# Optimization experiments

Hardware: AMD Instinct MI355X
Metric: run time of the kernel (lower is better)

The kernel has to match this reference:

```python
import jax, jax.numpy as jnp
import numpy as np

CAPACITY = 1_000_000
IN_FEATURES = 64
OUT_FEATURES = 64


def setup_inputs() -> dict:
    key = jax.random.key(0)
    k1, k2, k3 = jax.random.split(key, 3)
    query = jax.random.normal(k1, (IN_FEATURES,), dtype=jnp.float32)
    keys = jax.random.normal(k2, (CAPACITY, IN_FEATURES), dtype=jnp.float32)
    values = jax.random.normal(k3, (CAPACITY, OUT_FEATURES), dtype=jnp.float32)
    return {"query": query, "keys": keys, "values": values}


def reference(query, keys, values):
    # attention: [capacity] = keys [C, Din] @ query [Din]
    scores = keys @ query
    attention = jax.nn.softmax(scores, axis=0)
    # out: [Dout] = attention [C] @ values [C, Dout]
    out = attention @ values
    # usage-tracking argmax (softmax is monotone, argmax of scores == argmax of attention)
    amax = jnp.argmax(scores)
    return out, amax
```

## Files before the change

kernel.cpp:

```cpp
#include <hip/hip_runtime.h>
#include <math.h>

#define C_CAP 1000000
#define DIM 64

#define SCORES_OFF 0
#define P1_OFF     1000000
#define HDR_OFF    1010000
#define ACC_OFF    1010064

#define NB1 1024
#define NW1 (NB1 * 4)
#define NT64 (C_CAP / 64)
#define NB3 2048
#define NW3 (NB3 * 4)
#define NCHUNKS (C_CAP / 64)

__global__ __launch_bounds__(256, 4) void nd_scores(
    const float* __restrict__ query,
    const float* __restrict__ keys,
    float* __restrict__ ws, int ntiles, int stride)
{
    const int tid  = threadIdx.x;
    const int lane = tid & 63;
    const int wave = tid >> 6;
    const int wglobal = blockIdx.x * 4 + wave;

    float qs[64];
    #pragma unroll
    for (int j = 0; j < 64; ++j)
        qs[j] = __uint_as_float(__builtin_amdgcn_readfirstlane(__float_as_uint(query[j])));

    float m = -1e30f, l = 0.f;

    for (int t = wglobal; t < ntiles; t += stride) {
        const float4* __restrict__ kp =
            (const float4*)(keys + ((size_t)t * 64 + lane) * 64);

        float a0 = 0.f, a1 = 0.f, a2 = 0.f, a3 = 0.f;
        #pragma unroll
        for (int j = 0; j < 16; ++j) {
            const float4 k = kp[j];
            a0 = fmaf(k.x, qs[4 * j + 0], a0);
            a1 = fmaf(k.y, qs[4 * j + 1], a1);
            a2 = fmaf(k.z, qs[4 * j + 2], a2);
            a3 = fmaf(k.w, qs[4 * j + 3], a3);
        }
        const float s = (a0 + a1) + (a2 + a3);

        ws[SCORES_OFF + t * 64 + lane] = s;
        l += __expf(s);
        m = fmaxf(m, s);
    }

    #pragma unroll
    for (int off = 1; off <= 32; off <<= 1) {
        l += __shfl_xor(l, off);
        m = fmaxf(m, __shfl_xor(m, off));
    }

    __shared__ float s_m[4], s_l[4];
    if (lane == 0) { s_m[wave] = m; s_l[wave] = l; }
    __syncthreads();
    if (tid == 0) {
        float bm = s_m[0], bl = s_l[0];
        #pragma unroll
        for (int wv = 1; wv < 4; ++wv) {
            bl += s_l[wv];
            bm = fmaxf(bm, s_m[wv]);
        }
        float* bp = ws + P1_OFF + (size_t)blockIdx.x * 4;
        bp[0] = bm;
        bp[1] = bl;
    }
}

__global__ __launch_bounds__(256) void nd_reduce(float* __restrict__ ws, int nb)
{
    const int tid = threadIdx.x;
    float m = -1e30f, l = 0.f;
    for (int b = tid; b < nb; b += 256) {
        const float* bp = ws + P1_OFF + (size_t)b * 4;
        l += bp[1];
        m = fmaxf(m, bp[0]);
    }
    __shared__ float sm[256], sl[256];
    sm[tid] = m; sl[tid] = l;
    __syncthreads();
    for (int s = 128; s > 0; s >>= 1) {
        if (tid < s) {
            sl[tid] += sl[tid + s];
            sm[tid] = fmaxf(sm[tid], sm[tid + s]);
        }
        __syncthreads();
    }
    if (tid == 0) {
        const float M = sm[0];
        ws[HDR_OFF + 0] = M;
        ws[HDR_OFF + 1] = sl[0] * __expf(-M);
        ((int*)ws)[HDR_OFF + 2] = 0;
    }
    if (tid < 64) ws[ACC_OFF + tid] = 0.f;
}

__global__ __launch_bounds__(256, 8) void nd_pv(
    const float* __restrict__ values,
    float* __restrict__ ws, int nchunks, int nwaves_total)
{
    const int tid  = threadIdx.x;
    const int lane = tid & 63;
    const int wave = tid >> 6;
    const int wglobal = blockIdx.x * 4 + wave;

    const float M   = ws[HDR_OFF];
    const float thr = M - 23.0f;
    float acc = 0.f;

    for (int c = wglobal; c < nchunks; c += nwaves_total) {
        const float s = ws[SCORES_OFF + (size_t)c * 64 + lane];
        unsigned long long mask = __ballot(s > thr);
        if (mask) {
            if (s == M) ((int*)ws)[HDR_OFF + 2] = c * 64 + lane;
            const float w = __expf(s - M);
            while (mask) {
                const int b = __ffsll((long long)mask) - 1;
                mask &= mask - 1;
                const float wb = __shfl(w, b);
                acc = fmaf(wb, values[(size_t)(c * 64 + b) * 64 + lane], acc);
            }
        }
    }

    __shared__ float sA[4][64];
    sA[wave][lane] = acc;
    __syncthreads();
    if (tid < 64) {
        const float v = sA[0][tid] + sA[1][tid] + sA[2][tid] + sA[3][tid];
        if (v != 0.f) atomicAdd(ws + ACC_OFF + tid, v);
    }
}

__global__ __launch_bounds__(128) void nd_final(
    const float* __restrict__ ws, float* __restrict__ out)
{
    const int tid = threadIdx.x;
    if (tid < 64) out[tid] = ws[ACC_OFF + tid] / ws[HDR_OFF + 1];
    if (tid == 64) out[64] = (float)((const int*)ws)[HDR_OFF + 2];
}

extern "C" void kernel_launch(void* const* d_in, const int* in_sizes, int n_in,
                              void* d_out, int out_size, void* d_ws, size_t ws_size,
                              hipStream_t stream) {
    const float* query  = (const float*)d_in[0];
    const float* keys   = (const float*)d_in[1];
    const float* values = (const float*)d_in[2];
    float* out = (float*)d_out;
    float* ws  = (float*)d_ws;

    nd_scores<<<NB1, 256, 0, stream>>>(query, keys, ws, NT64, NW1);
    nd_reduce<<<1, 256, 0, stream>>>(ws, NB1);
    nd_pv<<<NB3, 256, 0, stream>>>(values, ws, NCHUNKS, NW3);
    nd_final<<<1, 128, 0, stream>>>(ws, out);
}
```

Before: 486.0 us.

## Coalesce key loads with 16-lane row groups and shuffle reductions in scores kernel

The scores kernel changes from one key row per lane, where each lane reads its own 256-byte row with strided float4 loads, to 16-lane groups that split a row across lanes. Each wave now covers 16 rows per tile with fully coalesced nontemporal float4 loads, then reduces the partial dot products with xor shuffles. The grid doubles and the occupancy hint rises to 8, and the per-lane query register array is replaced by one float4. The trade is extra shuffle work and redundant exp/max computation in every group, plus predicated score stores.

```diff
diff --git a/kernel.cpp b/kernel.cpp
--- a/kernel.cpp
+++ b/kernel.cpp
@@ -9,14 +9,16 @@
 #define HDR_OFF    1010000
 #define ACC_OFF    1010064
 
-#define NB1 1024
+#define NB1 2048
 #define NW1 (NB1 * 4)
-#define NT64 (C_CAP / 64)
+#define NTILES (C_CAP / 16)
 #define NB3 2048
 #define NW3 (NB3 * 4)
 #define NCHUNKS (C_CAP / 64)
 
-__global__ __launch_bounds__(256, 4) void nd_scores(
+typedef float f4 __attribute__((ext_vector_type(4)));
+
+__global__ __launch_bounds__(256, 8) void nd_scores(
     const float* __restrict__ query,
     const float* __restrict__ keys,
     float* __restrict__ ws, int ntiles, int stride)
@@ -24,40 +26,45 @@
     const int tid  = threadIdx.x;
     const int lane = tid & 63;
     const int wave = tid >> 6;
+    const int cl   = lane & 15;
+    const int g    = lane >> 4;
     const int wglobal = blockIdx.x * 4 + wave;
 
-    float qs[64];
-    #pragma unroll
-    for (int j = 0; j < 64; ++j)
-        qs[j] = __uint_as_float(__builtin_amdgcn_readfirstlane(__float_as_uint(query[j])));
+    const float4 q4 = ((const float4*)query)[cl];
+    const f4* __restrict__ k4p = (const f4*)keys;
 
     float m = -1e30f, l = 0.f;
 
     for (int t = wglobal; t < ntiles; t += stride) {
-        const float4* __restrict__ kp =
-            (const float4*)(keys + ((size_t)t * 64 + lane) * 64);
+        const f4* __restrict__ kp = k4p + (size_t)t * 256 + lane;
+        const f4 k0 = __builtin_nontemporal_load(kp);
+        const f4 k1 = __builtin_nontemporal_load(kp + 64);
+        const f4 k2 = __builtin_nontemporal_load(kp + 128);
+        const f4 k3 = __builtin_nontemporal_load(kp + 192);
 
-        float a0 = 0.f, a1 = 0.f, a2 = 0.f, a3 = 0.f;
-        #pragma unroll
-        for (int j = 0; j < 16; ++j) {
-            const float4 k = kp[j];
-            a0 = fmaf(k.x, qs[4 * j + 0], a0);
-            a1 = fmaf(k.y, qs[4 * j + 1], a1);
-            a2 = fmaf(k.z, qs[4 * j + 2], a2);
-            a3 = fmaf(k.w, qs[4 * j + 3], a3);
-        }
-        const float s = (a0 + a1) + (a2 + a3);
+        float s0 = fmaf(k0.x, q4.x, fmaf(k0.y, q4.y, fmaf(k0.z, q4.z, k0.w * q4.w)));
+        float s1 = fmaf(k1.x, q4.x, fmaf(k1.y, q4.y, fmaf(k1.z, q4.z, k1.w * q4.w)));
+        float s2 = fmaf(k2.x, q4.x, fmaf(k2.y, q4.y, fmaf(k2.z, q4.z, k2.w * q4.w)));
+        float s3 = fmaf(k3.x, q4.x, fmaf(k3.y, q4.y, fmaf(k3.z, q4.z, k3.w * q4.w)));
 
-        ws[SCORES_OFF + t * 64 + lane] = s;
-        l += __expf(s);
-        m = fmaxf(m, s);
+        s0 += __shfl_xor(s0, 1); s1 += __shfl_xor(s1, 1);
+        s2 += __shfl_xor(s2, 1); s3 += __shfl_xor(s3, 1);
+        s0 += __shfl_xor(s0, 2); s1 += __shfl_xor(s1, 2);
+        s2 += __shfl_xor(s2, 2); s3 += __shfl_xor(s3, 2);
+        s0 += __shfl_xor(s0, 4); s1 += __shfl_xor(s1, 4);
+        s2 += __shfl_xor(s2, 4); s3 += __shfl_xor(s3, 4);
+        s0 += __shfl_xor(s0, 8); s1 += __shfl_xor(s1, 8);
+        s2 += __shfl_xor(s2, 8); s3 += __shfl_xor(s3, 8);
+
+        const float sv = (cl == 0) ? s0 : (cl == 1) ? s1 : (cl == 2) ? s2 : s3;
+        if (cl < 4) ws[SCORES_OFF + t * 16 + 4 * cl + g] = sv;
+
+        l += (__expf(s0) + __expf(s1)) + (__expf(s2) + __expf(s3));
+        m = fmaxf(m, fmaxf(fmaxf(s0, s1), fmaxf(s2, s3)));
     }
 
-    #pragma unroll
-    for (int off = 1; off <= 32; off <<= 1) {
-        l += __shfl_xor(l, off);
-        m = fmaxf(m, __shfl_xor(m, off));
-    }
+    l += __shfl_xor(l, 16); m = fmaxf(m, __shfl_xor(m, 16));
+    l += __shfl_xor(l, 32); m = fmaxf(m, __shfl_xor(m, 32));
 
     __shared__ float s_m[4], s_l[4];
     if (lane == 0) { s_m[wave] = m; s_l[wave] = l; }
@@ -157,7 +164,7 @@
     float* out = (float*)d_out;
     float* ws  = (float*)d_ws;
 
-    nd_scores<<<NB1, 256, 0, stream>>>(query, keys, ws, NT64, NW1);
+    nd_scores<<<NB1, 256, 0, stream>>>(query, keys, ws, NTILES, NW1);
     nd_reduce<<<1, 256, 0, stream>>>(ws, NB1);
     nd_pv<<<NB3, 256, 0, stream>>>(values, ws, NCHUNKS, NW3);
     nd_final<<<1, 128, 0, stream>>>(ws, out);
```

After: 462.7 us. -4.8%, faster.
